# Kernel optimization log

Hardware: AMD Instinct MI355X
Metric: run time of the kernel (lower is better)

The kernel has to match this reference:

```python
import jax, jax.numpy as jnp
import numpy as np

B, N = 128, 512            # graphs per batch, nodes (seq len) per graph
NODE_VOCAB, APP_VOCAB = 30000, 5000
D, R, K = 128, 512, 3      # embed_size, rec_embed dim, Chebyshev order
EPS = 1e-12


def setup_inputs() -> dict:
    key = jax.random.key(0)
    ks = jax.random.split(key, 8)
    return {
        # all tokens nonzero -> every position is a valid node (item > 0 filter passes)
        "input_seq": jax.random.randint(ks[0], (B, N), 1, NODE_VOCAB),
        "recd_token": jax.random.randint(ks[1], (B, N), 1, APP_VOCAB),
        "embed_table": jax.random.normal(ks[2], (NODE_VOCAB, D), jnp.float32) * 0.02,
        "rec_embed_table": jax.random.normal(ks[3], (APP_VOCAB, R), jnp.float32) * 0.02,
        "cheb_w1": jax.random.normal(ks[4], (K, D, D), jnp.float32) / np.sqrt(D),
        "cheb_b1": jnp.zeros((D,), jnp.float32),
        "cheb_w2": jax.random.normal(ks[5], (K, D, D), jnp.float32) / np.sqrt(D),
        "cheb_b2": jnp.zeros((D,), jnp.float32),
    }


def _prop_matrix(app_emb):
    """Per-sample scaled Laplacian L_hat = -D^{-1/2} A D^{-1/2}.

    app_emb: [B,N,R] (detached upstream, matching recd.detach() in the source).
    Adjacency: cosine-sim matrix, entries below the mean of the nonzero strict
    upper triangle zeroed. ChebConv receives edge_index only -> binary weights,
    self-loops removed, default lambda_max=2 -> L_hat = -A_norm.
    """
    app_feat = app_emb / jnp.maximum(
        jnp.linalg.norm(app_emb, axis=-1, keepdims=True), EPS)      # F.normalize dim=1
    A = jnp.einsum('bnr,bmr->bnm', app_feat, app_feat)              # [B,N,N]
    upper = jnp.triu(A, 1)
    cnt = jnp.sum(upper != 0, axis=(1, 2)).astype(A.dtype)
    mean = jnp.sum(upper, axis=(1, 2)) / jnp.maximum(cnt, 1.0)      # [B]
    A = jnp.where(A < mean[:, None, None], 0.0, A)
    adj = (A != 0).astype(A.dtype) * (1.0 - jnp.eye(N, dtype=A.dtype))  # binary, no self-loops
    deg = adj.sum(-1)                                               # [B,N]
    dinv = jnp.where(deg > 0, jax.lax.rsqrt(jnp.maximum(deg, EPS)), 0.0)
    return -(dinv[:, :, None] * adj * dinv[:, None, :])             # [B,N,N]


def _cheb(x, S, w, b):
    # Chebyshev recurrence T0=x, T1=Sx, T2=2S T1 - T0
    tx0 = x
    tx1 = jnp.einsum('bnm,bmd->bnd', S, tx0)
    tx2 = 2.0 * jnp.einsum('bnm,bmd->bnd', S, tx1) - tx0
    return (jnp.einsum('bnd,de->bne', tx0, w[0])
            + jnp.einsum('bnd,de->bne', tx1, w[1])
            + jnp.einsum('bnd,de->bne', tx2, w[2]) + b)


def reference(input_seq, recd_token, embed_table, rec_embed_table,
              cheb_w1, cheb_b1, cheb_w2, cheb_b2):
    app_emb = rec_embed_table[recd_token]                           # [B,N,R]
    # adjacency built from detached embeddings (recd.detach() in source)
    S = jax.lax.stop_gradient(_prop_matrix(jax.lax.stop_gradient(app_emb)))
    x = embed_table[input_seq]                                      # [B,N,D]
    x = jax.nn.relu(_cheb(x, S, cheb_w1, cheb_b1))
    x = jax.nn.relu(_cheb(x, S, cheb_w2, cheb_b2))
    out = jnp.concatenate([x, app_emb], axis=-1)                    # [B,N,D+R]
    return out.reshape(B * N, D + R)                                # Batch'ed node features
```

## Files before the change

### kernel.cpp

```cpp
#include <hip/hip_runtime.h>
#include <hip/hip_bf16.h>

typedef __attribute__((ext_vector_type(8))) unsigned short ushort8;
typedef __attribute__((ext_vector_type(4))) unsigned short bf16x4;
typedef __attribute__((ext_vector_type(8))) short short8;
typedef __attribute__((ext_vector_type(4))) float f32x4;
typedef __attribute__((ext_vector_type(2))) unsigned long long u64x2;

#define DEV __device__ __forceinline__

DEV unsigned short f2bf(float f) {
    unsigned u = __builtin_bit_cast(unsigned, f);
    return (unsigned short)((u + 0x7fffu + ((u >> 16) & 1u)) >> 16);
}
DEV float bf2f(unsigned short h) {
    unsigned u = ((unsigned)h) << 16;
    return __builtin_bit_cast(float, u);
}
DEV float wred(float v) {
#pragma unroll
    for (int m = 32; m > 0; m >>= 1) v += __shfl_xor(v, m, 64);
    return v;
}

constexpr int N_ = 512, D_ = 128, R_ = 512;
constexpr long NN2 = (long)N_ * N_;

DEV void gll16(const void* g, void* l) {
    __builtin_amdgcn_global_load_lds(
        (const __attribute__((address_space(1))) unsigned*)g,
        (__attribute__((address_space(3))) unsigned*)l, 16, 0, 0);
}


__global__ __launch_bounds__(256) void k_gather_app(const int* __restrict__ recd,
                                                    const float* __restrict__ table,
                                                    float* __restrict__ out,
                                                    unsigned short* __restrict__ feat) {
    int tid = threadIdx.x, lane = tid & 63, w = tid >> 6;
    long r = (long)blockIdx.x * 4 + w;
    int tok = recd[r];
    const float* src = table + (long)tok * R_;
    int j = lane * 8;
    float4 v0 = *(const float4*)(src + j);
    float4 v1 = *(const float4*)(src + j + 4);
    float ssq = v0.x*v0.x + v0.y*v0.y + v0.z*v0.z + v0.w*v0.w
              + v1.x*v1.x + v1.y*v1.y + v1.z*v1.z + v1.w*v1.w;
    ssq = wred(ssq);
    float sc = 1.0f / fmaxf(sqrtf(ssq), 1e-12f);
    float* o = out + r * 640 + 128 + j;
    *(float4*)o = v0;
    *(float4*)(o + 4) = v1;
    ushort8 u;
    u[0]=f2bf(v0.x*sc); u[1]=f2bf(v0.y*sc); u[2]=f2bf(v0.z*sc); u[3]=f2bf(v0.w*sc);
    u[4]=f2bf(v1.x*sc); u[5]=f2bf(v1.y*sc); u[6]=f2bf(v1.z*sc); u[7]=f2bf(v1.w*sc);
    *(ushort8*)(feat + r * R_ + j) = u;
}

__global__ __launch_bounds__(256) void k_gather_x(const int* __restrict__ seq,
                                                  const float* __restrict__ table,
                                                  unsigned short* __restrict__ x) {
    long e8 = ((long)blockIdx.x * 256 + threadIdx.x) * 8;
    long r = e8 >> 7;
    int d0 = (int)(e8 & 127);
    int tok = seq[r];
    const float* src = table + (long)tok * D_ + d0;
    float4 v0 = *(const float4*)src, v1 = *(const float4*)(src + 4);
    ushort8 u;
    u[0]=f2bf(v0.x); u[1]=f2bf(v0.y); u[2]=f2bf(v0.z); u[3]=f2bf(v0.w);
    u[4]=f2bf(v1.x); u[5]=f2bf(v1.y); u[6]=f2bf(v1.z); u[7]=f2bf(v1.w);
    *(ushort8*)(x + e8) = u;
}

__global__ __launch_bounds__(256) void k_wT(const float* __restrict__ w1,
                                            const float* __restrict__ w2,
                                            unsigned short* __restrict__ wT) {
    int o = blockIdx.x * 256 + threadIdx.x;
    int l = o / 49152;
    int rr = o - l * 49152;
    int mat = rr >> 14;
    int e2 = rr & 16383;
    int e = e2 >> 7, d = e2 & 127;
    const float* w = l ? w2 : w1;
    float v;
    if (mat == 0)      v = w[d * 128 + e] - w[32768 + d * 128 + e];
    else if (mat == 1) v = w[16384 + d * 128 + e];
    else               v = 2.0f * w[32768 + d * 128 + e];
    wT[o] = f2bf(v);
}

__global__ __launch_bounds__(256) void k_trs(const unsigned short* __restrict__ in,
                                             const float* __restrict__ dinv,
                                             unsigned short* __restrict__ out) {
    __shared__ unsigned short t[64 * 128];
    int b = blockIdx.x >> 3, tn = blockIdx.x & 7;
    const unsigned short* ib = in + ((long)b * 512 + tn * 64) * 128;
    unsigned short* ob = out + (long)b * 65536 + tn * 64;
    int tid = threadIdx.x;
#pragma unroll
    for (int i = 0; i < 4; ++i) {
        int u = i * 256 + tid;
        int n = u >> 4, g = u & 15;
        float s = dinv[(long)b * 512 + tn * 64 + n];
        ushort8 v = *(const ushort8*)(ib + n * 128 + g * 8);
        ushort8 sv;
#pragma unroll
        for (int tt = 0; tt < 8; ++tt) sv[tt] = f2bf(bf2f(v[tt]) * s);
        int gs = g ^ ((n >> 3) & 7);
        *(ushort8*)(t + n * 128 + gs * 8) = sv;
    }
    __syncthreads();
#pragma unroll
    for (int i = 0; i < 4; ++i) {
        int u = i * 256 + tid;
        int d = u >> 3, n8 = (u & 7) * 8;
        ushort8 v;
#pragma unroll
        for (int tt = 0; tt < 8; ++tt) {
            int n = n8 + tt;
            int g = (d >> 3) ^ ((n >> 3) & 7);
            v[tt] = t[n * 128 + g * 8 + (d & 7)];
        }
        *(ushort8*)(ob + (long)d * 512 + n8) = v;
    }
}


DEV void stage_rowmajor(const unsigned short* base, long ld, int k0,
                        unsigned short* dst, int tid) {
#pragma unroll
    for (int i = 0; i < 4; ++i) {
        int u = i * 256 + tid;
        int r = u >> 3, c = (u & 7) * 8;
        gll16(base + (long)r * ld + k0 + c,
              dst + i * 2048 + (tid & 448) * 8);
    }
}

DEV void gemm_bt_core(const unsigned short* Abase, long ldA,
                      const unsigned short* Bbase, long ldB, int K,
                      unsigned short* As, unsigned short* Bs,
                      f32x4 acc[4][4]) {
    int tid = threadIdx.x, lane = tid & 63, wave = tid >> 6;
    int wm = wave >> 1, wn = wave & 1;
    int fr = lane & 15, ko = (lane >> 4) * 8;
    for (int k0 = 0; k0 < K; k0 += 64) {
        __syncthreads();
        stage_rowmajor(Abase, ldA, k0, As, tid);
        stage_rowmajor(Bbase, ldB, k0, Bs, tid);
        __syncthreads();
#pragma unroll
        for (int ks = 0; ks < 2; ++ks) {
            short8 a[4], b[4];
#pragma unroll
            for (int m = 0; m < 4; ++m)
                a[m] = *(const short8*)(As + (wm * 64 + m * 16 + fr) * 64 + ks * 32 + ko);
#pragma unroll
            for (int n = 0; n < 4; ++n)
                b[n] = *(const short8*)(Bs + (wn * 64 + n * 16 + fr) * 64 + ks * 32 + ko);
#pragma unroll
            for (int m = 0; m < 4; ++m)
#pragma unroll
                for (int n = 0; n < 4; ++n)
                    acc[m][n] = __builtin_amdgcn_mfma_f32_16x16x32_bf16(
                        a[m], b[n], acc[m][n], 0, 0, 0);
        }
    }
}


__global__ __launch_bounds__(256) void k_adj(const unsigned short* __restrict__ feat,
                                             unsigned short* __restrict__ Abf,
                                             float* __restrict__ psum,
                                             float* __restrict__ pcnt) {
    __shared__ unsigned short As[128 * 64], Bs[128 * 64];
    __shared__ float sred[4], cred[4];
    int g = blockIdx.x;
    int r = g & 7, q = g >> 3;
    int q10 = q / 10;
    int b = r + (q10 << 3);
    int t = q - q10 * 10;
    int tm = (t < 4) ? 0 : (t < 7) ? 1 : (t < 9) ? 2 : 3;
    int tn = t - (tm * (9 - tm)) / 2 + tm;
    const unsigned short* fb = feat + (long)b * NN2;
    f32x4 acc[4][4] = {};
    gemm_bt_core(fb + (long)tm * 128 * R_, R_, fb + (long)tn * 128 * R_, R_, R_,
                 As, Bs, acc);
    int tid = threadIdx.x, lane = tid & 63, wave = tid >> 6;
    int wm = wave >> 1, wn = wave & 1;
    float s = 0.f, c = 0.f;
    unsigned short* Ab = Abf + (long)b * NN2;
    bool diag = (tm == tn);
#pragma unroll
    for (int m = 0; m < 4; ++m)
#pragma unroll
        for (int n = 0; n < 4; ++n) {
            f32x4 v = acc[m][n];
            int gj = tn * 128 + wn * 64 + n * 16 + (lane & 15);
            int gi0 = tm * 128 + wm * 64 + m * 16 + (lane >> 4) * 4;
            bf16x4 tw;
#pragma unroll
            for (int qq = 0; qq < 4; ++qq) {
                int gi = gi0 + qq;
                unsigned short bv = f2bf(v[qq]);
                Ab[(long)gi * N_ + gj] = bv;
                tw[qq] = bv;
                if (gj > gi) {
                    s += v[qq];
                    c += (v[qq] != 0.0f) ? 1.0f : 0.0f;
                }
            }
            if (!diag)
                *(bf16x4*)(Ab + (long)gj * N_ + gi0) = tw;
        }
    s = wred(s);
    c = wred(c);
    if (lane == 0) { sred[wave] = s; cred[wave] = c; }
    __syncthreads();
    if (tid == 0) {
        psum[b * 16 + t] = sred[0] + sred[1] + sred[2] + sred[3];
        pcnt[b * 16 + t] = cred[0] + cred[1] + cred[2] + cred[3];
    }
}

__global__ __launch_bounds__(256) void k_degmask(unsigned short* __restrict__ Abf,
                                                 const float* __restrict__ psum,
                                                 const float* __restrict__ pcnt,
                                                 float* __restrict__ dinv) {
    __shared__ unsigned char mb[4][64];
    int tid = threadIdx.x, lane = tid & 63, w = tid >> 6;
    long r = (long)blockIdx.x * 4 + w;
    int b = (int)(r >> 9), i = (int)(r & 511);
    float s = 0.f, c = 0.f;
#pragma unroll
    for (int t = 0; t < 10; ++t) { s += psum[b * 16 + t]; c += pcnt[b * 16 + t]; }
    float m = s / fmaxf(c, 1.0f);
    const unsigned short* row = Abf + r * 512;
    ushort8 v = *(const ushort8*)(row + lane * 8);
    unsigned byt = 0;
    int cnt = 0;
#pragma unroll
    for (int t = 0; t < 8; ++t) {
        float f = bf2f(v[t]);
        int j = lane * 8 + t;
        bool keep = (f >= m) && (f != 0.0f) && (j != i);
        byt |= (keep ? 1u : 0u) << t;
        cnt += keep ? 1 : 0;
    }
    mb[w][lane] = (unsigned char)byt;
    float fc = wred((float)cnt);
    __syncthreads();
    if (lane < 8) {
        unsigned long long mword = *(const unsigned long long*)&mb[w][lane * 8];
        *(unsigned long long*)((unsigned char*)Abf + r * 1024 + lane * 8) = mword;
    }
    if (lane == 8) dinv[r] = (fc > 0.f) ? rsqrtf(fc) : 0.f;
}

template <int WT>
__global__ __launch_bounds__(256) void k_sxm(const unsigned short* __restrict__ Abf,
                                             const float* __restrict__ dinv,
                                             const unsigned short* __restrict__ pT,
                                             unsigned short* __restrict__ outN,
                                             unsigned short* __restrict__ outT) {
    __shared__ __align__(16) unsigned short Bs[128 * 64];
    __shared__ __align__(8) unsigned short lut4[16 * 4];
    int tid = threadIdx.x, lane = tid & 63, wave = tid >> 6;
    if (tid < 16) {
        unsigned long long e = 0;
#pragma unroll
        for (int j = 0; j < 4; ++j)
            if ((tid >> j) & 1) e |= 0x3F80ull << (16 * j);
        *(unsigned long long*)(lut4 + tid * 4) = e;
    }
    int g = blockIdx.x;
    int r = g & 7, q = g >> 3;
    int b = r + ((q >> 2) << 3);
    int tm = q & 3;
    int wm = wave >> 1, wn = wave & 1;
    int fr = lane & 15, ko = (lane >> 4) * 8;
    const unsigned char* mbase = (const unsigned char*)Abf + (long)b * 524288;
    const unsigned short* pb = pT + (long)b * 65536;
    f32x4 acc[4][4] = {};
    for (int k0 = 0; k0 < 512; k0 += 64) {
        __syncthreads();
        stage_rowmajor(pb, 512, k0, Bs, tid);
        unsigned long long mw[4];
#pragma unroll
        for (int m = 0; m < 4; ++m) {
            int row = tm * 128 + wm * 64 + m * 16 + fr;
            mw[m] = *(const unsigned long long*)(mbase + (long)row * 1024 + (k0 >> 3));
        }
        __syncthreads();
#pragma unroll
        for (int ks = 0; ks < 2; ++ks) {
            short8 a4[4], b4[4];
#pragma unroll
            for (int m = 0; m < 4; ++m) {
                unsigned w32 = (unsigned)(mw[m] >> (ks * 32));
                unsigned byt = (w32 >> ko) & 255u;
                unsigned long long lo = *(const unsigned long long*)(lut4 + (byt & 15u) * 4);
                unsigned long long hi = *(const unsigned long long*)(lut4 + (byt >> 4) * 4);
                u64x2 tt; tt[0] = lo; tt[1] = hi;
                a4[m] = __builtin_bit_cast(short8, tt);
            }
#pragma unroll
            for (int n = 0; n < 4; ++n)
                b4[n] = *(const short8*)(Bs + (wn * 64 + n * 16 + fr) * 64 + ks * 32 + ko);
#pragma unroll
            for (int m = 0; m < 4; ++m)
#pragma unroll
                for (int n = 0; n < 4; ++n)
                    acc[m][n] = __builtin_amdgcn_mfma_f32_16x16x32_bf16(
                        a4[m], b4[n], acc[m][n], 0, 0, 0);
        }
    }
    unsigned short* on = outN + (long)b * 65536;
#pragma unroll
    for (int m = 0; m < 4; ++m) {
        int gi0 = tm * 128 + wm * 64 + m * 16 + ((lane >> 4) << 2);
        float4 dv = *(const float4*)(dinv + (long)b * 512 + gi0);
#pragma unroll
        for (int n = 0; n < 4; ++n) {
            int gj = wn * 64 + n * 16 + fr;
            bf16x4 tw;
#pragma unroll
            for (int qq = 0; qq < 4; ++qq) {
                float dq = (&dv.x)[qq];
                float t1v = -dq * acc[m][n][qq];
                on[(long)(gi0 + qq) * 128 + gj] = f2bf(t1v);
                tw[qq] = f2bf(dq * t1v);
            }
            if (WT)
                *(bf16x4*)(outT + (long)b * 65536 + (long)gj * 512 + gi0) = tw;
        }
    }
}

template <int LAYER>
__global__ __launch_bounds__(256) void k_proj(const unsigned short* __restrict__ t0,
                                              const unsigned short* __restrict__ t1,
                                              const unsigned short* __restrict__ u,
                                              const unsigned short* __restrict__ wT,
                                              const float* __restrict__ bias,
                                              const float* __restrict__ dinv,
                                              unsigned short* __restrict__ ybf,
                                              unsigned short* __restrict__ pTout,
                                              float* __restrict__ out) {
    __shared__ unsigned short As[128 * 64], Bs[128 * 64];
    long row0 = (long)blockIdx.x * 128;
    f32x4 acc[4][4] = {};
    gemm_bt_core(t0 + row0 * D_, D_, wT,          D_, D_, As, Bs, acc);
    gemm_bt_core(t1 + row0 * D_, D_, wT + 16384,  D_, D_, As, Bs, acc);
    gemm_bt_core(u  + row0 * D_, D_, wT + 32768,  D_, D_, As, Bs, acc);
    int tid = threadIdx.x, lane = tid & 63, wave = tid >> 6;
    int wm = wave >> 1, wn = wave & 1;
#pragma unroll
    for (int m = 0; m < 4; ++m) {
        long gr0 = row0 + wm * 64 + m * 16 + ((lane >> 4) << 2);
        float4 dv;
        if (LAYER == 1) dv = *(const float4*)(dinv + gr0);
#pragma unroll
        for (int n = 0; n < 4; ++n) {
            int gj = wn * 64 + n * 16 + (lane & 15);
            bf16x4 tw;
#pragma unroll
            for (int q = 0; q < 4; ++q) {
                long gr = gr0 + q;
                float v = fmaxf(acc[m][n][q] + bias[gj], 0.0f);
                if (LAYER == 1) {
                    ybf[gr * D_ + gj] = f2bf(v);
                    tw[q] = f2bf((&dv.x)[q] * v);
                } else {
                    out[gr * 640 + gj] = v;
                }
            }
            if (LAYER == 1)
                *(bf16x4*)(pTout + (gr0 >> 9) * 65536 + (long)gj * 512 + (gr0 & 511)) = tw;
        }
    }
}


extern "C" void kernel_launch(void* const* d_in, const int* in_sizes, int n_in,
                              void* d_out, int out_size, void* d_ws, size_t ws_size,
                              hipStream_t stream) {
    const int* seq    = (const int*)d_in[0];
    const int* recd   = (const int*)d_in[1];
    const float* etab = (const float*)d_in[2];
    const float* rtab = (const float*)d_in[3];
    const float* w1   = (const float*)d_in[4];
    const float* b1   = (const float*)d_in[5];
    const float* w2   = (const float*)d_in[6];
    const float* b2   = (const float*)d_in[7];
    float* out = (float*)d_out;
    char* ws = (char*)d_ws;

    if (ws_size < 151470592u) return;

    unsigned short* Abf  = (unsigned short*)(ws);
    unsigned short* feat = (unsigned short*)(ws + 67108864);
    unsigned short* pTa  = (unsigned short*)(ws + 67108864);
    unsigned short* pTb  = (unsigned short*)(ws + 83886080);
    unsigned short* t1   = (unsigned short*)(ws + 100663296);
    unsigned short* ub   = (unsigned short*)(ws + 117440512);
    unsigned short* xbf  = (unsigned short*)(ws + 134217728);
    unsigned short* wT   = (unsigned short*)(ws + 150994944);
    float* psum = (float*)(ws + 151191552);
    float* pcnt = (float*)(ws + 151199744);
    float* dinv = (float*)(ws + 151208448);

    k_wT<<<384, 256, 0, stream>>>(w1, w2, wT);
    k_gather_app<<<16384, 256, 0, stream>>>(recd, rtab, out, feat);
    k_gather_x<<<4096, 256, 0, stream>>>(seq, etab, xbf);
    k_adj<<<1280, 256, 0, stream>>>(feat, Abf, psum, pcnt);
    k_degmask<<<16384, 256, 0, stream>>>(Abf, psum, pcnt, dinv);
    k_trs<<<1024, 256, 0, stream>>>(xbf, dinv, pTa);
    k_sxm<1><<<512, 256, 0, stream>>>(Abf, dinv, pTa, t1, pTb);
    k_sxm<0><<<512, 256, 0, stream>>>(Abf, dinv, pTb, ub, nullptr);
    k_proj<1><<<512, 256, 0, stream>>>(xbf, t1, ub, wT, b1, dinv, xbf, pTa, nullptr);
    k_sxm<1><<<512, 256, 0, stream>>>(Abf, dinv, pTa, t1, pTb);
    k_sxm<0><<<512, 256, 0, stream>>>(Abf, dinv, pTb, ub, nullptr);
    k_proj<2><<<512, 256, 0, stream>>>(xbf, t1, ub, wT + 49152, b2, dinv, nullptr, nullptr, out);
}
```

Baseline: 269.9 us.

## Fuse front gathers, degree/transpose, and second propagation with projection

Merges the three gather/weight-prep kernels into one launch and fuses the degree-mask pass with the scaled transpose of x. Each layer's second S·T1 propagation now runs in the same kernel as the weight projection, keeping the intermediate in LDS instead of writing it to global memory. Diagonal adjacency tiles stage only one operand. This cuts launches and global round-trips but grows LDS use per block and serialises the degree pass into 16-row loops.

New measurement: 233.2 us. 1.16x faster.

```diff
diff --git a/kernel.cpp b/kernel.cpp
--- a/kernel.cpp
+++ b/kernel.cpp
@@ -33,95 +33,60 @@
 }
 
 
-__global__ __launch_bounds__(256) void k_gather_app(const int* __restrict__ recd,
-                                                    const float* __restrict__ table,
-                                                    float* __restrict__ out,
-                                                    unsigned short* __restrict__ feat) {
-    int tid = threadIdx.x, lane = tid & 63, w = tid >> 6;
-    long r = (long)blockIdx.x * 4 + w;
-    int tok = recd[r];
-    const float* src = table + (long)tok * R_;
-    int j = lane * 8;
-    float4 v0 = *(const float4*)(src + j);
-    float4 v1 = *(const float4*)(src + j + 4);
-    float ssq = v0.x*v0.x + v0.y*v0.y + v0.z*v0.z + v0.w*v0.w
-              + v1.x*v1.x + v1.y*v1.y + v1.z*v1.z + v1.w*v1.w;
-    ssq = wred(ssq);
-    float sc = 1.0f / fmaxf(sqrtf(ssq), 1e-12f);
-    float* o = out + r * 640 + 128 + j;
-    *(float4*)o = v0;
-    *(float4*)(o + 4) = v1;
-    ushort8 u;
-    u[0]=f2bf(v0.x*sc); u[1]=f2bf(v0.y*sc); u[2]=f2bf(v0.z*sc); u[3]=f2bf(v0.w*sc);
-    u[4]=f2bf(v1.x*sc); u[5]=f2bf(v1.y*sc); u[6]=f2bf(v1.z*sc); u[7]=f2bf(v1.w*sc);
-    *(ushort8*)(feat + r * R_ + j) = u;
-}
-
-__global__ __launch_bounds__(256) void k_gather_x(const int* __restrict__ seq,
-                                                  const float* __restrict__ table,
-                                                  unsigned short* __restrict__ x) {
-    long e8 = ((long)blockIdx.x * 256 + threadIdx.x) * 8;
-    long r = e8 >> 7;
-    int d0 = (int)(e8 & 127);
-    int tok = seq[r];
-    const float* src = table + (long)tok * D_ + d0;
-    float4 v0 = *(const float4*)src, v1 = *(const float4*)(src + 4);
-    ushort8 u;
-    u[0]=f2bf(v0.x); u[1]=f2bf(v0.y); u[2]=f2bf(v0.z); u[3]=f2bf(v0.w);
-    u[4]=f2bf(v1.x); u[5]=f2bf(v1.y); u[6]=f2bf(v1.z); u[7]=f2bf(v1.w);
-    *(ushort8*)(x + e8) = u;
-}
-
-__global__ __launch_bounds__(256) void k_wT(const float* __restrict__ w1,
-                                            const float* __restrict__ w2,
-                                            unsigned short* __restrict__ wT) {
-    int o = blockIdx.x * 256 + threadIdx.x;
-    int l = o / 49152;
-    int rr = o - l * 49152;
-    int mat = rr >> 14;
-    int e2 = rr & 16383;
-    int e = e2 >> 7, d = e2 & 127;
-    const float* w = l ? w2 : w1;
-    float v;
-    if (mat == 0)      v = w[d * 128 + e] - w[32768 + d * 128 + e];
-    else if (mat == 1) v = w[16384 + d * 128 + e];
-    else               v = 2.0f * w[32768 + d * 128 + e];
-    wT[o] = f2bf(v);
-}
-
-__global__ __launch_bounds__(256) void k_trs(const unsigned short* __restrict__ in,
-                                             const float* __restrict__ dinv,
-                                             unsigned short* __restrict__ out) {
-    __shared__ unsigned short t[64 * 128];
-    int b = blockIdx.x >> 3, tn = blockIdx.x & 7;
-    const unsigned short* ib = in + ((long)b * 512 + tn * 64) * 128;
-    unsigned short* ob = out + (long)b * 65536 + tn * 64;
-    int tid = threadIdx.x;
-#pragma unroll
-    for (int i = 0; i < 4; ++i) {
-        int u = i * 256 + tid;
-        int n = u >> 4, g = u & 15;
-        float s = dinv[(long)b * 512 + tn * 64 + n];
-        ushort8 v = *(const ushort8*)(ib + n * 128 + g * 8);
-        ushort8 sv;
-#pragma unroll
-        for (int tt = 0; tt < 8; ++tt) sv[tt] = f2bf(bf2f(v[tt]) * s);
-        int gs = g ^ ((n >> 3) & 7);
-        *(ushort8*)(t + n * 128 + gs * 8) = sv;
-    }
-    __syncthreads();
-#pragma unroll
-    for (int i = 0; i < 4; ++i) {
-        int u = i * 256 + tid;
-        int d = u >> 3, n8 = (u & 7) * 8;
-        ushort8 v;
-#pragma unroll
-        for (int tt = 0; tt < 8; ++tt) {
-            int n = n8 + tt;
-            int g = (d >> 3) ^ ((n >> 3) & 7);
-            v[tt] = t[n * 128 + g * 8 + (d & 7)];
-        }
-        *(ushort8*)(ob + (long)d * 512 + n8) = v;
+__global__ __launch_bounds__(256) void k_front(const int* __restrict__ recd,
+                                               const float* __restrict__ rtab,
+                                               const int* __restrict__ seq,
+                                               const float* __restrict__ etab,
+                                               const float* __restrict__ w1,
+                                               const float* __restrict__ w2,
+                                               float* __restrict__ out,
+                                               unsigned short* __restrict__ feat,
+                                               unsigned short* __restrict__ x,
+                                               unsigned short* __restrict__ wT) {
+    int bid = blockIdx.x, tid = threadIdx.x;
+    if (bid < 16384) {
+        int lane = tid & 63, w = tid >> 6;
+        long r = (long)bid * 4 + w;
+        int tok = recd[r];
+        const float* src = rtab + (long)tok * R_;
+        int j = lane * 8;
+        float4 v0 = *(const float4*)(src + j);
+        float4 v1 = *(const float4*)(src + j + 4);
+        float ssq = v0.x*v0.x + v0.y*v0.y + v0.z*v0.z + v0.w*v0.w
+                  + v1.x*v1.x + v1.y*v1.y + v1.z*v1.z + v1.w*v1.w;
+        ssq = wred(ssq);
+        float sc = 1.0f / fmaxf(sqrtf(ssq), 1e-12f);
+        float* o = out + r * 640 + 128 + j;
+        *(float4*)o = v0;
+        *(float4*)(o + 4) = v1;
+        ushort8 u;
+        u[0]=f2bf(v0.x*sc); u[1]=f2bf(v0.y*sc); u[2]=f2bf(v0.z*sc); u[3]=f2bf(v0.w*sc);
+        u[4]=f2bf(v1.x*sc); u[5]=f2bf(v1.y*sc); u[6]=f2bf(v1.z*sc); u[7]=f2bf(v1.w*sc);
+        *(ushort8*)(feat + r * R_ + j) = u;
+    } else if (bid < 20480) {
+        long e8 = ((long)(bid - 16384) * 256 + tid) * 8;
+        long r = e8 >> 7;
+        int d0 = (int)(e8 & 127);
+        int tok = seq[r];
+        const float* src = etab + (long)tok * D_ + d0;
+        float4 v0 = *(const float4*)src, v1 = *(const float4*)(src + 4);
+        ushort8 u;
+        u[0]=f2bf(v0.x); u[1]=f2bf(v0.y); u[2]=f2bf(v0.z); u[3]=f2bf(v0.w);
+        u[4]=f2bf(v1.x); u[5]=f2bf(v1.y); u[6]=f2bf(v1.z); u[7]=f2bf(v1.w);
+        *(ushort8*)(x + e8) = u;
+    } else {
+        int o = (bid - 20480) * 256 + tid;
+        int l = o / 49152;
+        int rr = o - l * 49152;
+        int mat = rr >> 14;
+        int e2 = rr & 16383;
+        int e = e2 >> 7, d = e2 & 127;
+        const float* w = l ? w2 : w1;
+        float v;
+        if (mat == 0)      v = w[d * 128 + e] - w[32768 + d * 128 + e];
+        else if (mat == 1) v = w[16384 + d * 128 + e];
+        else               v = 2.0f * w[32768 + d * 128 + e];
+        wT[o] = f2bf(v);
     }
 }
 
@@ -140,14 +105,15 @@
 DEV void gemm_bt_core(const unsigned short* Abase, long ldA,
                       const unsigned short* Bbase, long ldB, int K,
                       unsigned short* As, unsigned short* Bs,
-                      f32x4 acc[4][4]) {
+                      f32x4 acc[4][4], bool dual) {
     int tid = threadIdx.x, lane = tid & 63, wave = tid >> 6;
     int wm = wave >> 1, wn = wave & 1;
     int fr = lane & 15, ko = (lane >> 4) * 8;
+    const unsigned short* Bsrc = dual ? Bs : As;
     for (int k0 = 0; k0 < K; k0 += 64) {
         __syncthreads();
         stage_rowmajor(Abase, ldA, k0, As, tid);
-        stage_rowmajor(Bbase, ldB, k0, Bs, tid);
+        if (dual) stage_rowmajor(Bbase, ldB, k0, Bs, tid);
         __syncthreads();
 #pragma unroll
         for (int ks = 0; ks < 2; ++ks) {
@@ -157,7 +123,7 @@
                 a[m] = *(const short8*)(As + (wm * 64 + m * 16 + fr) * 64 + ks * 32 + ko);
 #pragma unroll
             for (int n = 0; n < 4; ++n)
-                b[n] = *(const short8*)(Bs + (wn * 64 + n * 16 + fr) * 64 + ks * 32 + ko);
+                b[n] = *(const short8*)(Bsrc + (wn * 64 + n * 16 + fr) * 64 + ks * 32 + ko);
 #pragma unroll
             for (int m = 0; m < 4; ++m)
 #pragma unroll
@@ -182,15 +148,15 @@
     int t = q - q10 * 10;
     int tm = (t < 4) ? 0 : (t < 7) ? 1 : (t < 9) ? 2 : 3;
     int tn = t - (tm * (9 - tm)) / 2 + tm;
+    bool diag = (tm == tn);
     const unsigned short* fb = feat + (long)b * NN2;
     f32x4 acc[4][4] = {};
     gemm_bt_core(fb + (long)tm * 128 * R_, R_, fb + (long)tn * 128 * R_, R_, R_,
-                 As, Bs, acc);
+                 As, Bs, acc, !diag);
     int tid = threadIdx.x, lane = tid & 63, wave = tid >> 6;
     int wm = wave >> 1, wn = wave & 1;
     float s = 0.f, c = 0.f;
     unsigned short* Ab = Abf + (long)b * NN2;
-    bool diag = (tm == tn);
 #pragma unroll
     for (int m = 0; m < 4; ++m)
 #pragma unroll
@@ -223,41 +189,81 @@
     }
 }
 
-__global__ __launch_bounds__(256) void k_degmask(unsigned short* __restrict__ Abf,
-                                                 const float* __restrict__ psum,
-                                                 const float* __restrict__ pcnt,
-                                                 float* __restrict__ dinv) {
+__global__ __launch_bounds__(256) void k_degtrs(unsigned short* __restrict__ Abf,
+                                                const float* __restrict__ psum,
+                                                const float* __restrict__ pcnt,
+                                                const unsigned short* __restrict__ xin,
+                                                float* __restrict__ dinv,
+                                                unsigned short* __restrict__ pT) {
     __shared__ unsigned char mb[4][64];
+    __shared__ float sdinv[64];
+    __shared__ unsigned short t[64 * 128];
+    int bid = blockIdx.x;
+    int b = bid >> 3, tn = bid & 7;
     int tid = threadIdx.x, lane = tid & 63, w = tid >> 6;
-    long r = (long)blockIdx.x * 4 + w;
-    int b = (int)(r >> 9), i = (int)(r & 511);
     float s = 0.f, c = 0.f;
 #pragma unroll
-    for (int t = 0; t < 10; ++t) { s += psum[b * 16 + t]; c += pcnt[b * 16 + t]; }
+    for (int k = 0; k < 10; ++k) { s += psum[b * 16 + k]; c += pcnt[b * 16 + k]; }
     float m = s / fmaxf(c, 1.0f);
-    const unsigned short* row = Abf + r * 512;
-    ushort8 v = *(const ushort8*)(row + lane * 8);
-    unsigned byt = 0;
-    int cnt = 0;
-#pragma unroll
-    for (int t = 0; t < 8; ++t) {
-        float f = bf2f(v[t]);
-        int j = lane * 8 + t;
-        bool keep = (f >= m) && (f != 0.0f) && (j != i);
-        byt |= (keep ? 1u : 0u) << t;
-        cnt += keep ? 1 : 0;
-    }
-    mb[w][lane] = (unsigned char)byt;
-    float fc = wred((float)cnt);
+#pragma unroll 1
+    for (int i = 0; i < 16; ++i) {
+        int rl = w * 16 + i;
+        long r = (long)b * 512 + tn * 64 + rl;
+        int ig = tn * 64 + rl;
+        ushort8 v = *(const ushort8*)(Abf + r * 512 + lane * 8);
+        unsigned byt = 0;
+        int cnt = 0;
+#pragma unroll
+        for (int k = 0; k < 8; ++k) {
+            float f = bf2f(v[k]);
+            int j = lane * 8 + k;
+            bool keep = (f >= m) && (f != 0.0f) && (j != ig);
+            byt |= (keep ? 1u : 0u) << k;
+            cnt += keep ? 1 : 0;
+        }
+        mb[w][lane] = (unsigned char)byt;
+        float fc = wred((float)cnt);
+        if (lane < 8) {
+            unsigned long long mword = *(const unsigned long long*)&mb[w][lane * 8];
+            *(unsigned long long*)((unsigned char*)Abf + r * 1024 + lane * 8) = mword;
+        }
+        if (lane == 8) {
+            float dv = (fc > 0.f) ? rsqrtf(fc) : 0.f;
+            dinv[r] = dv;
+            sdinv[rl] = dv;
+        }
+    }
     __syncthreads();
-    if (lane < 8) {
-        unsigned long long mword = *(const unsigned long long*)&mb[w][lane * 8];
-        *(unsigned long long*)((unsigned char*)Abf + r * 1024 + lane * 8) = mword;
-    }
-    if (lane == 8) dinv[r] = (fc > 0.f) ? rsqrtf(fc) : 0.f;
-}
-
-template <int WT>
+    const unsigned short* ib = xin + ((long)b * 512 + tn * 64) * 128;
+    unsigned short* ob = pT + (long)b * 65536 + tn * 64;
+#pragma unroll
+    for (int i = 0; i < 4; ++i) {
+        int u = i * 256 + tid;
+        int n = u >> 4, g = u & 15;
+        float sc = sdinv[n];
+        ushort8 v = *(const ushort8*)(ib + n * 128 + g * 8);
+        ushort8 sv;
+#pragma unroll
+        for (int tt = 0; tt < 8; ++tt) sv[tt] = f2bf(bf2f(v[tt]) * sc);
+        int gs = g ^ ((n >> 3) & 7);
+        *(ushort8*)(t + n * 128 + gs * 8) = sv;
+    }
+    __syncthreads();
+#pragma unroll
+    for (int i = 0; i < 4; ++i) {
+        int u = i * 256 + tid;
+        int d = u >> 3, n8 = (u & 7) * 8;
+        ushort8 v;
+#pragma unroll
+        for (int tt = 0; tt < 8; ++tt) {
+            int n = n8 + tt;
+            int g = (d >> 3) ^ ((n >> 3) & 7);
+            v[tt] = t[n * 128 + g * 8 + (d & 7)];
+        }
+        *(ushort8*)(ob + (long)d * 512 + n8) = v;
+    }
+}
+
 __global__ __launch_bounds__(256) void k_sxm(const unsigned short* __restrict__ Abf,
                                              const float* __restrict__ dinv,
                                              const unsigned short* __restrict__ pT,
@@ -331,30 +337,114 @@
                 on[(long)(gi0 + qq) * 128 + gj] = f2bf(t1v);
                 tw[qq] = f2bf(dq * t1v);
             }
-            if (WT)
-                *(bf16x4*)(outT + (long)b * 65536 + (long)gj * 512 + gi0) = tw;
+            *(bf16x4*)(outT + (long)b * 65536 + (long)gj * 512 + gi0) = tw;
         }
     }
 }
 
 template <int LAYER>
-__global__ __launch_bounds__(256) void k_proj(const unsigned short* __restrict__ t0,
-                                              const unsigned short* __restrict__ t1,
-                                              const unsigned short* __restrict__ u,
-                                              const unsigned short* __restrict__ wT,
-                                              const float* __restrict__ bias,
-                                              const float* __restrict__ dinv,
-                                              unsigned short* __restrict__ ybf,
-                                              unsigned short* __restrict__ pTout,
-                                              float* __restrict__ out) {
-    __shared__ unsigned short As[128 * 64], Bs[128 * 64];
-    long row0 = (long)blockIdx.x * 128;
-    f32x4 acc[4][4] = {};
-    gemm_bt_core(t0 + row0 * D_, D_, wT,          D_, D_, As, Bs, acc);
-    gemm_bt_core(t1 + row0 * D_, D_, wT + 16384,  D_, D_, As, Bs, acc);
-    gemm_bt_core(u  + row0 * D_, D_, wT + 32768,  D_, D_, As, Bs, acc);
+__global__ __launch_bounds__(256) void k_sxp(const unsigned short* __restrict__ Abf,
+                                             const float* __restrict__ dinv,
+                                             const unsigned short* __restrict__ pTin,
+                                             const unsigned short* __restrict__ t0,
+                                             const unsigned short* __restrict__ t1,
+                                             const unsigned short* __restrict__ wTl,
+                                             const float* __restrict__ bias,
+                                             unsigned short* __restrict__ ybf,
+                                             unsigned short* __restrict__ pTout,
+                                             float* __restrict__ out) {
+    __shared__ __align__(16) unsigned short As[128 * 64], Bs[128 * 64];
+    __shared__ __align__(16) unsigned short uLds[128 * 132];
+    __shared__ __align__(8) unsigned short lut4[16 * 4];
     int tid = threadIdx.x, lane = tid & 63, wave = tid >> 6;
+    if (tid < 16) {
+        unsigned long long e = 0;
+#pragma unroll
+        for (int j = 0; j < 4; ++j)
+            if ((tid >> j) & 1) e |= 0x3F80ull << (16 * j);
+        *(unsigned long long*)(lut4 + tid * 4) = e;
+    }
+    int g = blockIdx.x;
+    int r = g & 7, q = g >> 3;
+    int b = r + ((q >> 2) << 3);
+    int tm = q & 3;
     int wm = wave >> 1, wn = wave & 1;
+    int fr = lane & 15, ko = (lane >> 4) * 8;
+    {
+        const unsigned char* mbase = (const unsigned char*)Abf + (long)b * 524288;
+        const unsigned short* pb = pTin + (long)b * 65536;
+        f32x4 acc[4][4] = {};
+        for (int k0 = 0; k0 < 512; k0 += 64) {
+            __syncthreads();
+            stage_rowmajor(pb, 512, k0, Bs, tid);
+            unsigned long long mw[4];
+#pragma unroll
+            for (int m = 0; m < 4; ++m) {
+                int row = tm * 128 + wm * 64 + m * 16 + fr;
+                mw[m] = *(const unsigned long long*)(mbase + (long)row * 1024 + (k0 >> 3));
+            }
+            __syncthreads();
+#pragma unroll
+            for (int ks = 0; ks < 2; ++ks) {
+                short8 a4[4], b4[4];
+#pragma unroll
+                for (int m = 0; m < 4; ++m) {
+                    unsigned w32 = (unsigned)(mw[m] >> (ks * 32));
+                    unsigned byt = (w32 >> ko) & 255u;
+                    unsigned long long lo = *(const unsigned long long*)(lut4 + (byt & 15u) * 4);
+                    unsigned long long hi = *(const unsigned long long*)(lut4 + (byt >> 4) * 4);
+                    u64x2 tt; tt[0] = lo; tt[1] = hi;
+                    a4[m] = __builtin_bit_cast(short8, tt);
+                }
+#pragma unroll
+                for (int n = 0; n < 4; ++n)
+                    b4[n] = *(const short8*)(Bs + (wn * 64 + n * 16 + fr) * 64 + ks * 32 + ko);
+#pragma unroll
+                for (int m = 0; m < 4; ++m)
+#pragma unroll
+                    for (int n = 0; n < 4; ++n)
+                        acc[m][n] = __builtin_amdgcn_mfma_f32_16x16x32_bf16(
+                            a4[m], b4[n], acc[m][n], 0, 0, 0);
+            }
+        }
+#pragma unroll
+        for (int m = 0; m < 4; ++m) {
+            int li0 = wm * 64 + m * 16 + ((lane >> 4) << 2);
+            float4 dv = *(const float4*)(dinv + (long)b * 512 + tm * 128 + li0);
+#pragma unroll
+            for (int n = 0; n < 4; ++n) {
+                int gj = wn * 64 + n * 16 + fr;
+#pragma unroll
+                for (int qq = 0; qq < 4; ++qq)
+                    uLds[(li0 + qq) * 132 + gj] = f2bf(-(&dv.x)[qq] * acc[m][n][qq]);
+            }
+        }
+    }
+    long row0 = (long)b * 512 + tm * 128;
+    f32x4 acc2[4][4] = {};
+    gemm_bt_core(t0 + row0 * D_, D_, wTl,          D_, D_, As, Bs, acc2, true);
+    gemm_bt_core(t1 + row0 * D_, D_, wTl + 16384,  D_, D_, As, Bs, acc2, true);
+    for (int s2 = 0; s2 < 2; ++s2) {
+        __syncthreads();
+        stage_rowmajor(wTl + 32768, 128, s2 * 64, Bs, tid);
+        __syncthreads();
+#pragma unroll
+        for (int ks = 0; ks < 2; ++ks) {
+            short8 a[4], bfr[4];
+#pragma unroll
+            for (int m = 0; m < 4; ++m)
+                a[m] = *(const short8*)(uLds + (wm * 64 + m * 16 + fr) * 132 + s2 * 64 + ks * 32 + ko);
+#pragma unroll
+            for (int n = 0; n < 4; ++n)
+                bfr[n] = *(const short8*)(Bs + (wn * 64 + n * 16 + fr) * 64 + ks * 32 + ko);
+#pragma unroll
+            for (int m = 0; m < 4; ++m)
+#pragma unroll
+                for (int n = 0; n < 4; ++n)
+                    acc2[m][n] = __builtin_amdgcn_mfma_f32_16x16x32_bf16(
+                        a[m], bfr[n], acc2[m][n], 0, 0, 0);
+        }
+    }
 #pragma unroll
     for (int m = 0; m < 4; ++m) {
         long gr0 = row0 + wm * 64 + m * 16 + ((lane >> 4) << 2);
@@ -365,12 +455,12 @@
             int gj = wn * 64 + n * 16 + (lane & 15);
             bf16x4 tw;
 #pragma unroll
-            for (int q = 0; q < 4; ++q) {
-                long gr = gr0 + q;
-                float v = fmaxf(acc[m][n][q] + bias[gj], 0.0f);
+            for (int qq = 0; qq < 4; ++qq) {
+                long gr = gr0 + qq;
+                float v = fmaxf(acc2[m][n][qq] + bias[gj], 0.0f);
                 if (LAYER == 1) {
                     ybf[gr * D_ + gj] = f2bf(v);
-                    tw[q] = f2bf((&dv.x)[q] * v);
+                    tw[qq] = f2bf((&dv.x)[qq] * v);
                 } else {
                     out[gr * 640 + gj] = v;
                 }
@@ -403,23 +493,19 @@
     unsigned short* pTa  = (unsigned short*)(ws + 67108864);
     unsigned short* pTb  = (unsigned short*)(ws + 83886080);
     unsigned short* t1   = (unsigned short*)(ws + 100663296);
-    unsigned short* ub   = (unsigned short*)(ws + 117440512);
     unsigned short* xbf  = (unsigned short*)(ws + 134217728);
     unsigned short* wT   = (unsigned short*)(ws + 150994944);
     float* psum = (float*)(ws + 151191552);
     float* pcnt = (float*)(ws + 151199744);
     float* dinv = (float*)(ws + 151208448);
 
-    k_wT<<<384, 256, 0, stream>>>(w1, w2, wT);
-    k_gather_app<<<16384, 256, 0, stream>>>(recd, rtab, out, feat);
-    k_gather_x<<<4096, 256, 0, stream>>>(seq, etab, xbf);
+    k_front<<<20864, 256, 0, stream>>>(recd, rtab, seq, etab, w1, w2, out, feat, xbf, wT);
     k_adj<<<1280, 256, 0, stream>>>(feat, Abf, psum, pcnt);
-    k_degmask<<<16384, 256, 0, stream>>>(Abf, psum, pcnt, dinv);
-    k_trs<<<1024, 256, 0, stream>>>(xbf, dinv, pTa);
-    k_sxm<1><<<512, 256, 0, stream>>>(Abf, dinv, pTa, t1, pTb);
-    k_sxm<0><<<512, 256, 0, stream>>>(Abf, dinv, pTb, ub, nullptr);
-    k_proj<1><<<512, 256, 0, stream>>>(xbf, t1, ub, wT, b1, dinv, xbf, pTa, nullptr);
-    k_sxm<1><<<512, 256, 0, stream>>>(Abf, dinv, pTa, t1, pTb);
-    k_sxm<0><<<512, 256, 0, stream>>>(Abf, dinv, pTb, ub, nullptr);
-    k_proj<2><<<512, 256, 0, stream>>>(xbf, t1, ub, wT + 49152, b2, dinv, nullptr, nullptr, out);
-}
+    k_degtrs<<<1024, 256, 0, stream>>>(Abf, psum, pcnt, xbf, dinv, pTa);
+    k_sxm<<<512, 256, 0, stream>>>(Abf, dinv, pTa, t1, pTb);
+    k_sxp<1><<<512, 256, 0, stream>>>(Abf, dinv, pTb, xbf, t1, wT, b1,
+                                      xbf, pTa, nullptr);
+    k_sxm<<<512, 256, 0, stream>>>(Abf, dinv, pTa, t1, pTb);
+    k_sxp<2><<<512, 256, 0, stream>>>(Abf, dinv, pTb, xbf, t1, wT + 49152, b2,
+                                      nullptr, nullptr, out);
+}
```
